# Kernel optimization log

Measured on AMD Instinct MI355X. Metric: run time of the kernel, lower is better.

Reference implementation:

```python
import jax, jax.numpy as jnp
import numpy as np

K = 50          # NEC paper uses p=50 neighbors
DELTA = 1e-3    # kernel smoothing constant


def setup_inputs() -> dict:
    key = jax.random.key(0)
    ks = jax.random.split(key, 8)
    B, D_IN, D, A, C = 512, 2, 128, 3, 200000
    s = lambda fan_in: 1.0 / np.sqrt(fan_in)
    return {
        "x": jax.random.normal(ks[0], (B, D_IN), jnp.float32),
        "W1": jax.random.normal(ks[1], (D_IN, D), jnp.float32) * s(D_IN),
        "b1": jnp.zeros((D,), jnp.float32),
        "W2": jax.random.normal(ks[2], (D, D), jnp.float32) * s(D),
        "b2": jnp.zeros((D,), jnp.float32),
        "W3": jax.random.normal(ks[3], (D, D), jnp.float32) * s(D),
        "b3": jnp.zeros((D,), jnp.float32),
        "W4": jax.random.normal(ks[4], (D, D), jnp.float32) * s(D),
        "b4": jnp.zeros((D,), jnp.float32),
        "keys": jax.random.normal(ks[5], (A, C, D), jnp.float32),
        "mem_values": jax.random.normal(ks[6], (A, C), jnp.float32),
    }


def _encode(x, W1, b1, W2, b2, W3, b3, W4, b4):
    h = jax.nn.relu(x @ W1 + b1)
    h = jax.nn.relu(h @ W2 + b2)
    h = jax.nn.relu(h @ W3 + b3)
    return h @ W4 + b4  # [B, D]


def _dnd_lookup(h, keys, mem_values):
    # h: [B, D]; keys: [A, C, D]; mem_values: [A, C]
    q2 = jnp.sum(h * h, axis=-1)                       # [B]
    k2 = jnp.sum(keys * keys, axis=-1)                 # [A, C]
    cross = jnp.einsum("bd,acd->bac", h, keys)         # [B, A, C]
    d2 = jnp.maximum(q2[:, None, None] + k2[None] - 2.0 * cross, 0.0)
    neg_d, idx = jax.lax.top_k(-d2, K)                  # [B, A, K]
    d_top = -neg_d
    w = 1.0 / (d_top + DELTA)                           # NEC kernel
    w = w / jnp.sum(w, axis=-1, keepdims=True)
    a_idx = jnp.arange(keys.shape[0])[None, :, None]    # [1, A, 1]
    v_top = mem_values[a_idx, idx]                      # gather -> [B, A, K]
    values = jnp.sum(w * v_top, axis=-1)                # [B, A]
    return values


def reference(x, W1, b1, W2, b2, W3, b3, W4, b4, keys, mem_values):
    h = _encode(x, W1, b1, W2, b2, W3, b3, W4, b4)
    values = _dnd_lookup(h, keys, mem_values)
    actions = jnp.argmax(values, axis=-1)
    return values, actions
```

## Files before the change

kernel.cpp:

```cpp
#include <hip/hip_runtime.h>
#include <hip/hip_bf16.h>
#include <math.h>

#define B_    512
#define DIM   128
#define A_    3
#define C_    200000
#define K_    50
#define DELTA 1e-3

typedef __attribute__((ext_vector_type(8))) short bf16x8;
typedef __attribute__((ext_vector_type(4))) float f32x4;

#define NBIN_A 128
#define CAP_A  1024
#define NSEG_G 128
#define TPS_G  13
#define NT_G   1563
#define HSEG   16
#define CHPS   782
#define ROWCH  12500

#define AOFF_H64   0u
#define AOFF_H32   524288u
#define AOFF_HBF   786432u
#define AOFF_Q2    917504u
#define AOFF_HIST  919552u
#define AOFF_CNT   1705984u
#define AOFF_TAUB  1712128u
#define AOFF_V64   1718272u
#define AOFF_CAND  1730560u
#define AOFF_BINS  8022016u
#define NEED_A     (8022016ull + 307200000ull)

#define NBIN_B 192
#define CAP_B  768
#define BM_B   64
#define BN_B   128
#define TPC_B  16
#define CHUNK_B (TPC_B*BN_B)
#define NCH_B  ((C_ + CHUNK_B - 1)/CHUNK_B)

#define BOFF_H32   0u
#define BOFF_H64   262144u
#define BOFF_Q2    786432u
#define BOFF_K2    788480u
#define BOFF_HIST  3188480u
#define BOFF_TAU   4368128u
#define BOFF_CNT   4374272u
#define BOFF_V64   4380416u
#define BOFF_CAND  4392704u

static __device__ inline unsigned short f2bf(float x) {
    union { float f; unsigned u; } c; c.f = x;
    unsigned r = (c.u + 0x7FFFu + ((c.u >> 16) & 1u)) >> 16;
    return (unsigned short)r;
}
static __device__ inline unsigned pkbf(float a, float b) {
    __hip_bfloat162 t = __float22bfloat162_rn(make_float2(a, b));
    union { __hip_bfloat162 h; unsigned u; } cv; cv.h = t; return cv.u;
}

__global__ __launch_bounds__(128) void mlp_kernel(
    const float* __restrict__ x,
    const float* __restrict__ W1, const float* __restrict__ b1,
    const float* __restrict__ W2, const float* __restrict__ b2,
    const float* __restrict__ W3, const float* __restrict__ b3,
    const float* __restrict__ W4, const float* __restrict__ b4,
    float* __restrict__ h32, unsigned short* __restrict__ hbf,
    double* __restrict__ h64, float* __restrict__ q2)
{
    int b = blockIdx.x, t = threadIdx.x;
    __shared__ double s0[DIM], s1[DIM];
    double x0 = (double)x[b*2+0], x1 = (double)x[b*2+1];
    double h = x0*(double)W1[t] + x1*(double)W1[DIM+t] + (double)b1[t];
    s0[t] = h > 0.0 ? h : 0.0;
    __syncthreads();
    double acc = (double)b2[t];
    for (int k = 0; k < DIM; k++) acc += s0[k]*(double)W2[k*DIM+t];
    s1[t] = acc > 0.0 ? acc : 0.0;
    __syncthreads();
    acc = (double)b3[t];
    for (int k = 0; k < DIM; k++) acc += s1[k]*(double)W3[k*DIM+t];
    s0[t] = acc > 0.0 ? acc : 0.0;
    __syncthreads();
    acc = (double)b4[t];
    for (int k = 0; k < DIM; k++) acc += s0[k]*(double)W4[k*DIM+t];
    h64[b*DIM+t] = acc;
    float hf = (float)acc;
    h32[b*DIM+t] = hf;
    hbf[b*DIM+t] = f2bf(hf);
    s1[t] = acc*acc;
    __syncthreads();
    for (int s = 64; s > 0; s >>= 1) { if (t < s) s1[t] += s1[t+s]; __syncthreads(); }
    if (t == 0) q2[b] = (float)s1[0];
}

__global__ __launch_bounds__(256, 2) void gemm_bin_kernel(
    const float* __restrict__ keys, const unsigned short* __restrict__ hbf,
    const float* __restrict__ q2, unsigned char* __restrict__ bins)
{
    const int seg = blockIdx.x, my = blockIdx.y, a = blockIdx.z;
    const int b0 = my*128;
    const int tid = threadIdx.x;
    const int lane = tid & 63, w = tid >> 6;
    const int lm = lane & 15, kh = lane >> 4;
    const int wm = w & 1, wn = w >> 1;

    __shared__ short sA[128*136];
    __shared__ short sB[128*136];
    __shared__ float q2s[128];
    __shared__ float k2s[128];

    {
        int r = tid >> 1, hh = tid & 1;
        const int4* gp = (const int4*)hbf + (size_t)(b0 + r)*16 + hh*8;
        int4* dp = (int4*)&sA[r*136 + hh*64];
        #pragma unroll
        for (int q = 0; q < 8; q++) dp[q] = gp[q];
        if (tid < 128) q2s[tid] = q2[b0 + tid];
    }

    for (int t = 0; t < TPS_G; t++) {
        int nt = seg*TPS_G + t;
        if (nt >= NT_G) break;
        int n0 = nt*128;
        __syncthreads();
        {
            int r = tid >> 1, hh = tid & 1;
            int nr = n0 + r; if (nr >= C_) nr = C_-1;
            const float4* gp = (const float4*)(keys + ((size_t)a*C_ + nr)*128) + hh*16;
            float ss = 0.0f;
            int4* dp = (int4*)&sB[r*136 + hh*64];
            #pragma unroll
            for (int q = 0; q < 8; q++) {
                float4 v0 = gp[2*q], v1 = gp[2*q+1];
                ss += v0.x*v0.x + v0.y*v0.y + v0.z*v0.z + v0.w*v0.w
                    + v1.x*v1.x + v1.y*v1.y + v1.z*v1.z + v1.w*v1.w;
                int4 pk;
                pk.x = (int)pkbf(v0.x, v0.y);
                pk.y = (int)pkbf(v0.z, v0.w);
                pk.z = (int)pkbf(v1.x, v1.y);
                pk.w = (int)pkbf(v1.z, v1.w);
                dp[q] = pk;
            }
            ss += __shfl_xor(ss, 1, 64);
            if (hh == 0) k2s[r] = ss;
        }
        __syncthreads();

        f32x4 acc[4][4];
        #pragma unroll
        for (int i = 0; i < 4; i++)
            #pragma unroll
            for (int j = 0; j < 4; j++) acc[i][j] = (f32x4){0.f, 0.f, 0.f, 0.f};

        #pragma unroll
        for (int kst = 0; kst < 4; kst++) {
            bf16x8 af[4], bfv[4];
            #pragma unroll
            for (int i = 0; i < 4; i++)
                af[i] = *(const bf16x8*)&sA[(wm*64 + i*16 + lm)*136 + kst*32 + kh*8];
            #pragma unroll
            for (int j = 0; j < 4; j++)
                bfv[j] = *(const bf16x8*)&sB[(wn*64 + j*16 + lm)*136 + kst*32 + kh*8];
            #pragma unroll
            for (int i = 0; i < 4; i++)
                #pragma unroll
                for (int j = 0; j < 4; j++)
                    acc[i][j] = __builtin_amdgcn_mfma_f32_16x16x32_bf16(af[i], bfv[j], acc[i][j], 0, 0, 0);
        }

        unsigned char* bp = bins + ((size_t)(a*B_ + b0))*C_ + n0;
        #pragma unroll
        for (int j = 0; j < 4; j++) {
            int col = wn*64 + j*16 + lm;
            int n = n0 + col;
            if (n < C_) {
                float kk = k2s[col];
                #pragma unroll
                for (int i = 0; i < 4; i++) {
                    int rl = wm*64 + i*16 + kh*4;
                    #pragma unroll
                    for (int reg = 0; reg < 4; reg++) {
                        float d2v = q2s[rl+reg] + kk - 2.0f*acc[i][j][reg];
                        float dc = fminf(fmaxf(d2v, 16.0f), 4095.0f);
                        int bin = (int)(__float_as_uint(dc) >> 19) - 2096;
                        bp[(size_t)(rl+reg)*C_ + col] = (unsigned char)bin;
                    }
                }
            }
        }
    }
}

__global__ __launch_bounds__(256) void histA_kernel(const unsigned char* __restrict__ bins,
                                                    unsigned* __restrict__ hist)
{
    int q = blockIdx.x;
    int seg = blockIdx.y;
    int tid = threadIdx.x;
    int a = q >> 9, b = q & 511;
    int p = b*A_ + a;
    __shared__ unsigned hs[NBIN_A*8];
    for (int i = tid; i < NBIN_A*8; i += 256) hs[i] = 0;
    __syncthreads();
    const uint4* row = (const uint4*)(bins + (size_t)q*C_);
    int ch0 = seg*CHPS, ch1 = ch0 + CHPS; if (ch1 > ROWCH) ch1 = ROWCH;
    int rep = tid & 7;
    for (int ch = ch0 + tid; ch < ch1; ch += 256) {
        uint4 v = row[ch];
        unsigned d[4] = {v.x, v.y, v.z, v.w};
        #pragma unroll
        for (int e = 0; e < 4; e++) {
            unsigned x = d[e];
            atomicAdd(&hs[((x      ) & 127u)*8 + rep], 1u);
            atomicAdd(&hs[((x >>  8) & 127u)*8 + rep], 1u);
            atomicAdd(&hs[((x >> 16) & 127u)*8 + rep], 1u);
            atomicAdd(&hs[((x >> 24) & 127u)*8 + rep], 1u);
        }
    }
    __syncthreads();
    if (tid < NBIN_A) {
        unsigned s = 0;
        #pragma unroll
        for (int r2 = 0; r2 < 8; r2++) s += hs[tid*8 + r2];
        if (s) atomicAdd(&hist[(size_t)p*NBIN_A + tid], s);
    }
}

__global__ void tauA_kernel(const unsigned* __restrict__ hist, int* __restrict__ taubin)
{
    int p = blockIdx.x*256 + threadIdx.x;
    if (p >= B_*A_) return;
    const unsigned* hp = hist + (size_t)p*NBIN_A;
    unsigned cum = 0; int jsel = NBIN_A-1;
    for (int j = 0; j < NBIN_A; j++) { cum += hp[j]; if (cum >= K_) { jsel = j; break; } }
    unsigned c1 = cum + (jsel+1 < NBIN_A ? hp[jsel+1] : 0u);
    unsigned c2 = c1  + (jsel+2 < NBIN_A ? hp[jsel+2] : 0u);
    int jt = (c2 <= 768u) ? jsel+2 : jsel+1;
    if (jt > NBIN_A-1) jt = NBIN_A-1;
    taubin[p] = jt;
}

__global__ __launch_bounds__(256) void collectA_kernel(const unsigned char* __restrict__ bins,
    const int* __restrict__ taubin, unsigned* __restrict__ cnt, int* __restrict__ cand)
{
    int q = blockIdx.x, seg = blockIdx.y, tid = threadIdx.x;
    int a = q >> 9, b = q & 511;
    int p = b*A_ + a;
    int tb = taubin[p];
    unsigned thr  = (unsigned)(tb + 1);
    unsigned addv = (128u - thr) * 0x01010101u;
    const uint4* row = (const uint4*)(bins + (size_t)q*C_);
    int ch0 = seg*CHPS, ch1 = ch0 + CHPS; if (ch1 > ROWCH) ch1 = ROWCH;
    for (int ch = ch0 + tid; ch < ch1; ch += 256) {
        uint4 v = row[ch];
        unsigned d[4] = {v.x, v.y, v.z, v.w};
        #pragma unroll
        for (int e = 0; e < 4; e++) {
            unsigned m = (d[e] + addv) & 0x80808080u;
            if (m != 0x80808080u) {
                #pragma unroll
                for (int by = 0; by < 4; by++) {
                    if (!((m >> (8*by + 7)) & 1u)) {
                        int n = ch*16 + e*4 + by;
                        unsigned pos = atomicAdd(&cnt[p], 1u);
                        if (pos < CAP_A) cand[(size_t)p*CAP_A + pos] = n;
                    }
                }
            }
        }
    }
}

__global__ __launch_bounds__(256) void k2_kernel(const float* __restrict__ keys,
                                                 float* __restrict__ k2)
{
    int r = blockIdx.x*4 + (threadIdx.x >> 6);
    int lane = threadIdx.x & 63;
    float2 v = ((const float2*)keys)[(size_t)r*64 + lane];
    float s = v.x*v.x + v.y*v.y;
    #pragma unroll
    for (int off = 32; off > 0; off >>= 1) s += __shfl_down(s, off, 64);
    if (lane == 0) k2[r] = s;
}

template<int MODE>
__global__ __launch_bounds__(256) void pass_kernel(
    const float* __restrict__ keys, const float* __restrict__ h32,
    const float* __restrict__ q2,   const float* __restrict__ k2,
    unsigned* __restrict__ hist,    const float* __restrict__ tau,
    unsigned* __restrict__ cnt,     int* __restrict__ cand)
{
    const int bt = blockIdx.x;
    const int ch = blockIdx.y;
    const int a  = blockIdx.z;
    const int b0 = bt*BM_B;
    const int tid = threadIdx.x;
    const int tx = tid & 31, ty = tid >> 5;

    __shared__ float4 hs4[BM_B*33];
    __shared__ float4 ks4[BN_B*33];
    __shared__ float  q2s[BM_B];
    __shared__ float  taus[BM_B];
    __shared__ unsigned hist_s[MODE == 0 ? BM_B*NBIN_B : 1];

    #pragma unroll
    for (int q = 0; q < BM_B*32/256; q++) {
        int flat = q*256 + tid; int row = flat >> 5, kq = flat & 31;
        hs4[row*33 + kq] = ((const float4*)h32)[(size_t)(b0+row)*32 + kq];
    }
    if (tid < BM_B) {
        q2s[tid] = q2[b0+tid];
        if (MODE == 1) taus[tid] = tau[(b0+tid)*A_ + a];
    }
    if (MODE == 0) for (int i = tid; i < BM_B*NBIN_B; i += 256) hist_s[i] = 0;
    const float* __restrict__ k2g = k2 + (size_t)a*C_;

    for (int t = 0; t < TPC_B; t++) {
        int n0 = ch*CHUNK_B + t*BN_B;
        if (n0 >= C_) break;
        __syncthreads();
        #pragma unroll
        for (int q = 0; q < 16; q++) {
            int flat = q*256 + tid; int row = flat >> 5, kq = flat & 31;
            int nr = n0 + row; if (nr >= C_) nr = C_-1;
            ks4[row*33 + kq] = ((const float4*)keys)[((size_t)a*C_ + nr)*32 + kq];
        }
        __syncthreads();

        float acc[8][4];
        #pragma unroll
        for (int i = 0; i < 8; i++)
            #pragma unroll
            for (int j = 0; j < 4; j++) acc[i][j] = 0.0f;

        for (int kq = 0; kq < 32; kq++) {
            float4 hv[8], kv[4];
            #pragma unroll
            for (int i = 0; i < 8; i++) hv[i] = hs4[(ty*8+i)*33 + kq];
            #pragma unroll
            for (int j = 0; j < 4; j++) kv[j] = ks4[(j*32+tx)*33 + kq];
            #pragma unroll
            for (int i = 0; i < 8; i++)
                #pragma unroll
                for (int j = 0; j < 4; j++)
                    acc[i][j] += hv[i].x*kv[j].x + hv[i].y*kv[j].y
                               + hv[i].z*kv[j].z + hv[i].w*kv[j].w;
        }

        #pragma unroll
        for (int i = 0; i < 8; i++) {
            int bl = ty*8 + i;
            float q2b = q2s[bl];
            #pragma unroll
            for (int j = 0; j < 4; j++) {
                int n = n0 + j*32 + tx;
                if (n < C_) {
                    float d2f = fmaxf(q2b + k2g[n] - 2.0f*acc[i][j], 0.0f);
                    if (MODE == 0) {
                        int bin = (int)(__float_as_uint(d2f + 1.0f) >> 19) - 2032;
                        bin = bin < 0 ? 0 : (bin > NBIN_B-1 ? NBIN_B-1 : bin);
                        atomicAdd(&hist_s[bl*NBIN_B + bin], 1u);
                    } else {
                        if (d2f < taus[bl]) {
                            int p = (b0+bl)*A_ + a;
                            unsigned pos = atomicAdd(&cnt[p], 1u);
                            if (pos < CAP_B) cand[(size_t)p*CAP_B + pos] = n;
                        }
                    }
                }
            }
        }
    }
    if (MODE == 0) {
        __syncthreads();
        for (int i = tid; i < BM_B*NBIN_B; i += 256) {
            unsigned v = hist_s[i];
            if (v) {
                int bl = i / NBIN_B, bin = i % NBIN_B;
                atomicAdd(&hist[(size_t)((b0+bl)*A_ + a)*NBIN_B + bin], v);
            }
        }
    }
}

__global__ __launch_bounds__(256) void tauB_kernel(const unsigned* __restrict__ hist,
                                                   float* __restrict__ tau)
{
    int p = blockIdx.x*256 + threadIdx.x;
    if (p >= B_*A_) return;
    const unsigned* hp = hist + (size_t)p*NBIN_B;
    unsigned cum = 0; int jsel = NBIN_B-1;
    for (int j = 0; j < NBIN_B; j++) { cum += hp[j]; if (cum >= K_) { jsel = j; break; } }
    tau[p] = __uint_as_float((unsigned)(2034 + jsel) << 19) - 1.0f;
}

__global__ __launch_bounds__(256) void select_kernel(
    const float* __restrict__ keys, const double* __restrict__ h64,
    const float* __restrict__ mem_values,
    const unsigned* __restrict__ cnt, const int* __restrict__ cand,
    float* __restrict__ out_values, double* __restrict__ val64, int cap)
{
    int p = blockIdx.x; int b = p / A_, a = p % A_;
    int tid = threadIdx.x;
    __shared__ double hd[DIM];
    __shared__ double d2s[CAP_A];
    __shared__ float  vs[CAP_A];
    __shared__ double red[256];
    __shared__ int    redi[256];
    __shared__ double acc_w, acc_wv;

    for (int i = tid; i < DIM; i += 256) hd[i] = h64[(size_t)b*DIM + i];
    if (tid == 0) { acc_w = 0.0; acc_wv = 0.0; }
    __syncthreads();

    int n = (int)cnt[p]; if (n > cap) n = cap;
    for (int i = tid; i < n; i += 256) {
        int c = cand[(size_t)p*cap + i];
        const float4* kr = (const float4*)(keys + ((size_t)a*C_ + c)*DIM);
        double s0 = 0.0, s1 = 0.0;
        #pragma unroll 4
        for (int kq = 0; kq < 32; kq++) {
            float4 kv = kr[kq];
            double d0 = hd[4*kq+0] - (double)kv.x;
            double d1 = hd[4*kq+1] - (double)kv.y;
            double d2 = hd[4*kq+2] - (double)kv.z;
            double d3 = hd[4*kq+3] - (double)kv.w;
            s0 += d0*d0 + d1*d1; s1 += d2*d2 + d3*d3;
        }
        d2s[i] = s0 + s1;
        vs[i]  = mem_values[(size_t)a*C_ + c];
    }
    __syncthreads();

    int kk = n < K_ ? n : K_;
    for (int t = 0; t < kk; t++) {
        double best = 1e300; int bi = -1;
        for (int i = tid; i < n; i += 256)
            if (d2s[i] < best) { best = d2s[i]; bi = i; }
        red[tid] = best; redi[tid] = bi;
        __syncthreads();
        for (int s = 128; s > 0; s >>= 1) {
            if (tid < s && red[tid+s] < red[tid]) { red[tid] = red[tid+s]; redi[tid] = redi[tid+s]; }
            __syncthreads();
        }
        if (tid == 0) {
            int wi = redi[0];
            double d = d2s[wi]; if (d < 0.0) d = 0.0;
            double wgt = 1.0 / (d + DELTA);
            acc_w += wgt; acc_wv += wgt * (double)vs[wi];
            d2s[wi] = 2e300;
        }
        __syncthreads();
    }
    if (tid == 0) {
        double v = acc_wv / acc_w;
        out_values[p] = (float)v;
        val64[p] = v;
    }
}

__global__ void argmax_kernel(const double* __restrict__ val64, float* __restrict__ out)
{
    int b = blockIdx.x*blockDim.x + threadIdx.x;
    if (b >= B_) return;
    double v0 = val64[b*A_+0], v1 = val64[b*A_+1], v2 = val64[b*A_+2];
    int bi = 0; double bv = v0;
    if (v1 > bv) { bv = v1; bi = 1; }
    if (v2 > bv) { bv = v2; bi = 2; }
    out[B_*A_ + b] = (float)bi;
}

extern "C" void kernel_launch(void* const* d_in, const int* in_sizes, int n_in,
                              void* d_out, int out_size, void* d_ws, size_t ws_size,
                              hipStream_t stream)
{
    const float* x    = (const float*)d_in[0];
    const float* W1   = (const float*)d_in[1];
    const float* b1   = (const float*)d_in[2];
    const float* W2   = (const float*)d_in[3];
    const float* b2   = (const float*)d_in[4];
    const float* W3   = (const float*)d_in[5];
    const float* b3   = (const float*)d_in[6];
    const float* W4   = (const float*)d_in[7];
    const float* b4   = (const float*)d_in[8];
    const float* keys = (const float*)d_in[9];
    const float* memv = (const float*)d_in[10];

    char* ws = (char*)d_ws;

    if (ws_size >= NEED_A) {
        double*         h64  = (double*)        (ws + AOFF_H64);
        float*          h32  = (float*)         (ws + AOFF_H32);
        unsigned short* hbf  = (unsigned short*)(ws + AOFF_HBF);
        float*          q2   = (float*)         (ws + AOFF_Q2);
        unsigned*       hist = (unsigned*)      (ws + AOFF_HIST);
        unsigned*       cnt  = (unsigned*)      (ws + AOFF_CNT);
        int*            taub = (int*)           (ws + AOFF_TAUB);
        double*         v64  = (double*)        (ws + AOFF_V64);
        int*            cand = (int*)           (ws + AOFF_CAND);
        unsigned char*  bins = (unsigned char*) (ws + AOFF_BINS);

        hipMemsetAsync(ws + AOFF_HIST, 0, (AOFF_CNT + B_*A_*4) - AOFF_HIST, stream);

        mlp_kernel<<<B_, 128, 0, stream>>>(x, W1, b1, W2, b2, W3, b3, W4, b4, h32, hbf, h64, q2);
        gemm_bin_kernel<<<dim3(NSEG_G, 4, A_), 256, 0, stream>>>(keys, hbf, q2, bins);
        histA_kernel<<<dim3(B_*A_, HSEG), 256, 0, stream>>>(bins, hist);
        tauA_kernel<<<(B_*A_ + 255)/256, 256, 0, stream>>>(hist, taub);
        collectA_kernel<<<dim3(B_*A_, HSEG), 256, 0, stream>>>(bins, taub, cnt, cand);
        select_kernel<<<B_*A_, 256, 0, stream>>>(keys, h64, memv, cnt, cand, (float*)d_out, v64, CAP_A);
        argmax_kernel<<<2, 256, 0, stream>>>(v64, (float*)d_out);
    } else {
        float*          h32  = (float*)         (ws + BOFF_H32);
        double*         h64  = (double*)        (ws + BOFF_H64);
        float*          q2   = (float*)         (ws + BOFF_Q2);
        float*          k2   = (float*)         (ws + BOFF_K2);
        unsigned*       hist = (unsigned*)      (ws + BOFF_HIST);
        float*          tau  = (float*)         (ws + BOFF_TAU);
        unsigned*       cnt  = (unsigned*)      (ws + BOFF_CNT);
        double*         v64  = (double*)        (ws + BOFF_V64);
        int*            cand = (int*)           (ws + BOFF_CAND);
        unsigned short* hbf  = (unsigned short*)(ws + BOFF_CAND);

        hipMemsetAsync(ws + BOFF_HIST, 0, (BOFF_CNT + B_*A_*4) - BOFF_HIST, stream);

        mlp_kernel<<<B_, 128, 0, stream>>>(x, W1, b1, W2, b2, W3, b3, W4, b4, h32, hbf, h64, q2);
        k2_kernel<<<(A_*C_)/4, 256, 0, stream>>>(keys, k2);
        pass_kernel<0><<<dim3(B_/BM_B, NCH_B, A_), 256, 0, stream>>>(keys, h32, q2, k2, hist, nullptr, nullptr, nullptr);
        tauB_kernel<<<(B_*A_ + 255)/256, 256, 0, stream>>>(hist, tau);
        pass_kernel<1><<<dim3(B_/BM_B, NCH_B, A_), 256, 0, stream>>>(keys, h32, q2, k2, nullptr, tau, cnt, cand);
        select_kernel<<<B_*A_, 256, 0, stream>>>(keys, h64, memv, cnt, cand, (float*)d_out, v64, CAP_B);
        argmax_kernel<<<2, 256, 0, stream>>>(v64, (float*)d_out);
    }
}
```

Baseline: 1.060 ms.

## Prefetch key tiles into registers, pack byte stores, use wave-shuffle argmin

The GEMM-bin kernel now loads the next 128-row key tile into registers while the MFMA work on the current tile runs, overlapping global loads with compute. The MFMA operands are swapped so each lane holds four consecutive key columns, which lets the bin bytes be packed into a 32-bit word per store instead of four scattered byte stores. The select kernel replaces the shared-memory tree reduction for the argmin with 64-lane wave shuffles plus a 4-way final compare, cutting barriers per iteration. The prefetch costs 64 extra VGPRs, which may reduce occupancy under the 2-blocks launch bound.

```diff
diff --git a/kernel.cpp b/kernel.cpp
--- a/kernel.cpp
+++ b/kernel.cpp
@@ -107,6 +107,10 @@
     const int lm = lane & 15, kh = lane >> 4;
     const int wm = w & 1, wn = w >> 1;
 
+    int tc = NT_G - seg*TPS_G;
+    if (tc <= 0) return;
+    if (tc > TPS_G) tc = TPS_G;
+
     __shared__ short sA[128*136];
     __shared__ short sB[128*136];
     __shared__ float q2s[128];
@@ -121,20 +125,25 @@
         if (tid < 128) q2s[tid] = q2[b0 + tid];
     }
 
-    for (int t = 0; t < TPS_G; t++) {
-        int nt = seg*TPS_G + t;
-        if (nt >= NT_G) break;
-        int n0 = nt*128;
-        __syncthreads();
+    const int r = tid >> 1, hh = tid & 1;
+
+    float4 lv[16];
+    {
+        int nr = seg*TPS_G*128 + r; if (nr >= C_) nr = C_-1;
+        const float4* gp = (const float4*)(keys + ((size_t)a*C_ + nr)*128) + hh*16;
+        #pragma unroll
+        for (int q = 0; q < 16; q++) lv[q] = gp[q];
+    }
+
+    for (int t = 0; t < tc; t++) {
+        int n0 = (seg*TPS_G + t)*128;
+
         {
-            int r = tid >> 1, hh = tid & 1;
-            int nr = n0 + r; if (nr >= C_) nr = C_-1;
-            const float4* gp = (const float4*)(keys + ((size_t)a*C_ + nr)*128) + hh*16;
             float ss = 0.0f;
             int4* dp = (int4*)&sB[r*136 + hh*64];
             #pragma unroll
             for (int q = 0; q < 8; q++) {
-                float4 v0 = gp[2*q], v1 = gp[2*q+1];
+                float4 v0 = lv[2*q], v1 = lv[2*q+1];
                 ss += v0.x*v0.x + v0.y*v0.y + v0.z*v0.z + v0.w*v0.w
                     + v1.x*v1.x + v1.y*v1.y + v1.z*v1.z + v1.w*v1.w;
                 int4 pk;
@@ -149,6 +158,13 @@
         }
         __syncthreads();
 
+        if (t+1 < tc) {
+            int nn = n0 + 128 + r; if (nn >= C_) nn = C_-1;
+            const float4* gp = (const float4*)(keys + ((size_t)a*C_ + nn)*128) + hh*16;
+            #pragma unroll
+            for (int q = 0; q < 16; q++) lv[q] = gp[q];
+        }
+
         f32x4 acc[4][4];
         #pragma unroll
         for (int i = 0; i < 4; i++)
@@ -160,10 +176,10 @@
             bf16x8 af[4], bfv[4];
             #pragma unroll
             for (int i = 0; i < 4; i++)
-                af[i] = *(const bf16x8*)&sA[(wm*64 + i*16 + lm)*136 + kst*32 + kh*8];
+                af[i] = *(const bf16x8*)&sB[(wn*64 + i*16 + lm)*136 + kst*32 + kh*8];
             #pragma unroll
             for (int j = 0; j < 4; j++)
-                bfv[j] = *(const bf16x8*)&sB[(wn*64 + j*16 + lm)*136 + kst*32 + kh*8];
+                bfv[j] = *(const bf16x8*)&sA[(wm*64 + j*16 + lm)*136 + kst*32 + kh*8];
             #pragma unroll
             for (int i = 0; i < 4; i++)
                 #pragma unroll
@@ -173,24 +189,29 @@
 
         unsigned char* bp = bins + ((size_t)(a*B_ + b0))*C_ + n0;
         #pragma unroll
-        for (int j = 0; j < 4; j++) {
-            int col = wn*64 + j*16 + lm;
-            int n = n0 + col;
+        for (int i = 0; i < 4; i++) {
+            int nl = wn*64 + i*16 + kh*4;
+            int n = n0 + nl;
             if (n < C_) {
-                float kk = k2s[col];
+                float4 kq = *(const float4*)&k2s[nl];
                 #pragma unroll
-                for (int i = 0; i < 4; i++) {
-                    int rl = wm*64 + i*16 + kh*4;
+                for (int j = 0; j < 4; j++) {
+                    int bcol = wm*64 + j*16 + lm;
+                    float q2v = q2s[bcol];
+                    unsigned pk = 0;
                     #pragma unroll
-                    for (int reg = 0; reg < 4; reg++) {
-                        float d2v = q2s[rl+reg] + kk - 2.0f*acc[i][j][reg];
+                    for (int rg = 0; rg < 4; rg++) {
+                        float kv = (rg == 0) ? kq.x : (rg == 1) ? kq.y : (rg == 2) ? kq.z : kq.w;
+                        float d2v = (q2v + kv) - 2.0f*acc[i][j][rg];
                         float dc = fminf(fmaxf(d2v, 16.0f), 4095.0f);
-                        int bin = (int)(__float_as_uint(dc) >> 19) - 2096;
-                        bp[(size_t)(rl+reg)*C_ + col] = (unsigned char)bin;
+                        unsigned bin = (__float_as_uint(dc) >> 19) - 2096u;
+                        pk |= bin << (8*rg);
                     }
+                    *(unsigned*)(bp + (size_t)bcol*C_ + nl) = pk;
                 }
             }
         }
+        __syncthreads();
     }
 }
 
@@ -408,8 +429,8 @@
     __shared__ double hd[DIM];
     __shared__ double d2s[CAP_A];
     __shared__ float  vs[CAP_A];
-    __shared__ double red[256];
-    __shared__ int    redi[256];
+    __shared__ double redv[4];
+    __shared__ int    redi4[4];
     __shared__ double acc_w, acc_wv;
 
     for (int i = tid; i < DIM; i += 256) hd[i] = h64[(size_t)b*DIM + i];
@@ -440,14 +461,20 @@
         double best = 1e300; int bi = -1;
         for (int i = tid; i < n; i += 256)
             if (d2s[i] < best) { best = d2s[i]; bi = i; }
-        red[tid] = best; redi[tid] = bi;
-        __syncthreads();
-        for (int s = 128; s > 0; s >>= 1) {
-            if (tid < s && red[tid+s] < red[tid]) { red[tid] = red[tid+s]; redi[tid] = redi[tid+s]; }
-            __syncthreads();
-        }
+        #pragma unroll
+        for (int off = 32; off > 0; off >>= 1) {
+            double ov = __shfl_xor(best, off, 64);
+            int    oi = __shfl_xor(bi,   off, 64);
+            if (ov < best) { best = ov; bi = oi; }
+        }
+        int wv = tid >> 6;
+        if ((tid & 63) == 0) { redv[wv] = best; redi4[wv] = bi; }
+        __syncthreads();
         if (tid == 0) {
-            int wi = redi[0];
+            double bv = redv[0]; int wi = redi4[0];
+            if (redv[1] < bv) { bv = redv[1]; wi = redi4[1]; }
+            if (redv[2] < bv) { bv = redv[2]; wi = redi4[2]; }
+            if (redv[3] < bv) { bv = redv[3]; wi = redi4[3]; }
             double d = d2s[wi]; if (d < 0.0) d = 0.0;
             double wgt = 1.0 / (d + DELTA);
             acc_w += wgt; acc_wv += wgt * (double)vs[wi];
```

Result: slower. 1.124 ms (+6.0%).
